# Kernel optimization log

Hardware: AMD Instinct MI355X
Metric: run time of the kernel (lower is better)

The kernel has to match this reference:

```python
import jax, jax.numpy as jnp
import numpy as np
import math

N = 50000      # nodes (single node type 'mapping_var')
D = 128        # in_feats
R = 3          # relations
E = 800000     # edges per relation
OUT = 64
ALPHA = 0.5
BETA1 = math.log(2.0)    # log(lambda/layer + 1), layer=1, lambda=1
BETA2 = math.log(1.5)    # layer=2
SLOPE = 0.01             # leaky_relu default negative slope


def setup_inputs() -> dict:
    key = jax.random.key(0)
    ks = jax.random.split(key, 8)
    x = jax.random.normal(ks[0], (N, D), dtype=jnp.float32)
    src = jax.random.randint(ks[1], (R, E), 0, N, dtype=jnp.int32)
    dst = jax.random.randint(ks[2], (R, E), 0, N, dtype=jnp.int32)
    W1 = jax.random.normal(ks[3], (R, D, D), dtype=jnp.float32) * 0.05
    b1 = jnp.zeros((R, D), dtype=jnp.float32)
    W2 = jax.random.normal(ks[4], (R, D, D), dtype=jnp.float32) * 0.05
    b2 = jnp.zeros((R, D), dtype=jnp.float32)
    Wlin = jax.random.normal(ks[5], (D, OUT), dtype=jnp.float32) * 0.05
    blin = jnp.zeros((OUT,), dtype=jnp.float32)
    return {"x": x, "src": src, "dst": dst, "W1": W1, "b1": b1,
            "W2": W2, "b2": b2, "Wlin": Wlin, "blin": blin}


def _gcn2_rel(h, feat0, src, dst, W, b, beta, act):
    """One GCN2Conv on one relation. h,feat0: [N,D]; src,dst: [E]."""
    ones = jnp.ones(src.shape, h.dtype)
    deg_out = jnp.maximum(jax.ops.segment_sum(ones, src, num_segments=N), 1.0)
    deg_in = jnp.maximum(jax.ops.segment_sum(ones, dst, num_segments=N), 1.0)
    hs = h * (deg_out ** -0.5)[:, None]              # src-side normalize
    agg = jax.ops.segment_sum(hs[src], dst, num_segments=N)  # SpMM via gather+scatter
    feat = agg * (deg_in ** -0.5)[:, None]           # dst-side normalize
    rst = feat * (1.0 - ALPHA) + ALPHA * feat0       # initial-residual blend
    rst = (1.0 - beta) * rst + beta * (rst @ W) + b  # identity mapping (project_initial_features)
    if act:
        rst = jnp.where(rst >= 0, rst, SLOPE * rst)  # leaky_relu
    return rst


def reference(x, src, dst, W1, b1, W2, b2, Wlin, blin):
    # conv1: per-relation GCN2Conv(layer=1, leaky_relu), mean-aggregate over relations
    h1 = jax.vmap(lambda s, d, w, bb: _gcn2_rel(x, x, s, d, w, bb, BETA1, True))(
        src, dst, W1, b1).mean(axis=0)
    # dropout: eval-mode identity
    # conv2: per-relation GCN2Conv(layer=2, no activation), feat_0 = original inputs
    h2 = jax.vmap(lambda s, d, w, bb: _gcn2_rel(h1, x, s, d, w, bb, BETA2, False))(
        src, dst, W2, b2).mean(axis=0)
    return h2 @ Wlin + blin
```

## Files before the change

### kernel.cpp

```cpp
#include <hip/hip_runtime.h>

#define NN    50000
#define DD    128
#define RR    3
#define EE    800000
#define OUTD  64
#define BKT   128
#define NBK   391
#define CAP   2560
#define CAPB  2560
#define CHUNK 2048
#define NCH   391
#define NPB   3125
#define SETUPB 6250
#define ALPHA_ 0.5f
#define SLOPE_ 0.01f
#define BETA1_ 0.6931471805599453f
#define BETA2_ 0.4054651081081644f

typedef __attribute__((ext_vector_type(8))) short short8;
typedef __attribute__((ext_vector_type(4))) float f32x4;

__device__ __forceinline__ unsigned short f2b(float f) {
    unsigned int u = __builtin_bit_cast(unsigned int, f);
    u += 0x7FFFu + ((u >> 16) & 1u);
    return (unsigned short)(u >> 16);
}
__device__ __forceinline__ unsigned int pack2(float lo, float hi) {
    return (unsigned int)f2b(lo) | ((unsigned int)f2b(hi) << 16);
}
__device__ __forceinline__ float blo(unsigned int w) { return __builtin_bit_cast(float, w << 16); }
__device__ __forceinline__ float bhi(unsigned int w) { return __builtin_bit_cast(float, w & 0xFFFF0000u); }

__global__ __launch_bounds__(256) void bin_kernel(
    const int* __restrict__ src, const int* __restrict__ dst,
    int* __restrict__ bcnt_d, int* __restrict__ bcnt_s,
    int* __restrict__ pairs_d, unsigned short* __restrict__ pairs_s)
{
    __shared__ int hist[NBK];
    __shared__ int lbase[NBK];
    __shared__ int gdelta[NBK];
    __shared__ int lcur[NBK];
    __shared__ unsigned int staging[CHUNK];
    unsigned short* staging16 = (unsigned short*)staging;
    const int tid = threadIdx.x;
    const int blk = blockIdx.x;
    const int phase = (blk >= RR * NCH);
    const int rb = phase ? blk - RR * NCH : blk;
    const int r = rb / NCH;
    const int chunk = rb % NCH;
    const int e0 = chunk * CHUNK;
    const int n = min(CHUNK, EE - e0);
    const int* sp = src + (size_t)r * EE + e0;
    const int* dp = dst + (size_t)r * EE + e0;
    const int* kp = phase ? sp : dp;

    for (int i = tid; i < NBK; i += 256) hist[i] = 0;
    __syncthreads();
    for (int i = tid; i < n; i += 256)
        atomicAdd(&hist[kp[i] >> 7], 1);
    __syncthreads();
    if (tid < 64) {
        int carry = 0;
        for (int c0 = 0; c0 < NBK; c0 += 64) {
            const int idx = c0 + tid;
            const int v = (idx < NBK) ? hist[idx] : 0;
            int incl = v;
            #pragma unroll
            for (int d = 1; d < 64; d <<= 1) {
                const int t = __shfl_up(incl, d, 64);
                if (tid >= d) incl += t;
            }
            if (idx < NBK) lbase[idx] = carry + incl - v;
            carry += __shfl(incl, 63, 64);
        }
    }
    __syncthreads();
    if (!phase) {
        for (int b = tid; b < NBK; b += 256) {
            lcur[b] = lbase[b];
            const int h = hist[b];
            if (h > 0) {
                const int gstart = (r * NBK + b) * CAP + atomicAdd(&bcnt_d[r * NBK + b], h);
                gdelta[b] = gstart - lbase[b];
            }
        }
        __syncthreads();
        for (int i = tid; i < n; i += 256) {
            const int d = dp[i];
            const int b = d >> 7;
            const int pos = atomicAdd(&lcur[b], 1);
            staging[pos] = (unsigned int)sp[i] | ((unsigned int)(d & 127) << 16)
                         | ((unsigned int)b << 23);
        }
        __syncthreads();
        for (int j = tid; j < n; j += 256) {
            const unsigned int v = staging[j];
            const int b = v >> 23;
            const int gi = gdelta[b] + j;
            const int lo = gi - (r * NBK + b) * CAP;
            if (lo < CAP) pairs_d[gi] = (int)(v & 0x7FFFFF);
        }
    } else {
        for (int b = tid; b < NBK; b += 256) {
            lcur[b] = lbase[b];
            const int h = hist[b];
            if (h > 0) {
                const int gstart = (r * NBK + b) * CAPB + atomicAdd(&bcnt_s[r * NBK + b], h);
                gdelta[b] = gstart - lbase[b];
            }
        }
        __syncthreads();
        for (int i = tid; i < n; i += 256) {
            const int s = sp[i];
            const int b = s >> 7;
            const int pos = atomicAdd(&lcur[b], 1);
            staging16[pos] = (unsigned short)((b << 7) | (s & 127));
        }
        __syncthreads();
        for (int j = tid; j < n; j += 256) {
            const unsigned short v = staging16[j];
            const int b = v >> 7;
            const int gi = gdelta[b] + j;
            const int lo = gi - (r * NBK + b) * CAPB;
            if (lo < CAPB) pairs_s[gi] = v;
        }
    }
}

__global__ __launch_bounds__(256) void dego_setup_kernel(
    const unsigned short* __restrict__ pairs_s, const int* __restrict__ bcnt_s,
    float* __restrict__ dego_r,
    const float* __restrict__ x, unsigned short* __restrict__ xb,
    const float* __restrict__ W1, const float* __restrict__ W2,
    const float* __restrict__ Wlin, unsigned short* __restrict__ Wt1,
    unsigned short* __restrict__ Wt2, unsigned short* __restrict__ WlT)
{
    __shared__ int scnt[BKT];
    const int tid = threadIdx.x;
    const int blk = blockIdx.x;
    if (blk < RR * NBK) {
        const int n2 = min(bcnt_s[blk], CAPB);
        const unsigned short* ps = pairs_s + (size_t)blk * CAPB;
        if (tid < BKT) scnt[tid] = 0;
        __syncthreads();
        for (int i = tid; i < n2; i += 256)
            atomicAdd(&scnt[ps[i] & 127], 1);
        __syncthreads();
        if (tid < BKT) {
            const int r = blk / NBK;
            const int g = (blk % NBK) * BKT + tid;
            if (g < NN)
                dego_r[r * NN + g] = rsqrtf((float)max(scnt[tid], 1));
        }
    } else {
        const int i = (blk - RR * NBK) * 256 + tid;
        {
            const float4 v = ((const float4*)x)[i];
            ushort4 o;
            o.x = f2b(v.x); o.y = f2b(v.y); o.z = f2b(v.z); o.w = f2b(v.w);
            ((ushort4*)xb)[i] = o;
        }
        if (i < RR * DD * DD) {
            const int r = i >> 14, rem = i & 16383, nn = rem >> 7, k = rem & 127;
            const float diag = (k == nn) ? 1.0f : 0.0f;
            const float w1 = W1[r * DD * DD + k * DD + nn];
            Wt1[i] = f2b(BETA1_ * w1 + diag * (1.0f - BETA1_));
            const float w2 = W2[r * DD * DD + k * DD + nn];
            Wt2[i] = f2b((BETA2_ * w2 + diag * (1.0f - BETA2_)) * (1.0f / 3.0f));
        } else if (i < RR * DD * DD + OUTD * DD) {
            const int j = i - RR * DD * DD;
            const int nn = j >> 7, k = j & 127;
            WlT[j] = f2b(Wlin[k * OUTD + nn]);
        }
    }
}

__global__ __launch_bounds__(256) void sort_kernel(
    int* __restrict__ pairs_d, const int* __restrict__ bcnt_d,
    const float* __restrict__ dego_r,
    int* __restrict__ off_g, int* __restrict__ cnt_g, float* __restrict__ degi_r)
{
    __shared__ int stage[CAP];
    __shared__ int cnt[BKT];
    __shared__ int base[BKT];
    __shared__ int pos[BKT];
    const int tid = threadIdx.x;
    const int bid = blockIdx.x;
    const int rr = bid / NBK;
    const int n = min(bcnt_d[bid], CAP);
    int* pp = pairs_d + (size_t)bid * CAP;
    const float* dego = dego_r + (size_t)rr * NN;
    if (tid < BKT) cnt[tid] = 0;
    __syncthreads();
    for (int i = tid; i < n; i += 256) {
        const int p = pp[i];
        stage[i] = p;
        atomicAdd(&cnt[p >> 16], 1);
    }
    __syncthreads();
    if (tid < 64) {
        int carry = 0;
        for (int c0 = 0; c0 < BKT; c0 += 64) {
            const int v = cnt[c0 + tid];
            int incl = v;
            #pragma unroll
            for (int d = 1; d < 64; d <<= 1) {
                const int t = __shfl_up(incl, d, 64);
                if (tid >= d) incl += t;
            }
            base[c0 + tid] = carry + incl - v;
            carry += __shfl(incl, 63, 64);
        }
    }
    __syncthreads();
    if (tid < BKT) {
        pos[tid] = base[tid];
        const int g = (bid % NBK) * BKT + tid;
        if (g < NN) {
            off_g[rr * NN + g] = bid * CAP + base[tid];
            cnt_g[rr * NN + g] = cnt[tid];
            degi_r[rr * NN + g] = rsqrtf((float)max(cnt[tid], 1));
        }
    }
    __syncthreads();
    for (int i = tid; i < n; i += 256) {
        const int p = stage[i];
        const int q = atomicAdd(&pos[p >> 16], 1);
        const int s = p & 0xFFFF;
        pp[q] = s | ((int)f2b(dego[s]) << 16);
    }
}

__global__ __launch_bounds__(256) void pull_all_kernel(
    const unsigned short* __restrict__ hb,
    const unsigned short* __restrict__ xb,
    const int* __restrict__ csrw, const int* __restrict__ off_g,
    const int* __restrict__ cnt_g, const float* __restrict__ degi_r,
    unsigned short* __restrict__ aggb)
{
    const int blk = blockIdx.x;
    const int r = blk / NPB;
    const int node = (blk % NPB) * 16 + (threadIdx.x >> 4);
    const int lane = threadIdx.x & 15;
    const int gi = r * NN + node;
    const int j0 = off_g[gi];
    const int j1 = j0 + cnt_g[gi];
    const uint4* hb4 = (const uint4*)hb;
    float a0 = 0.f, a1 = 0.f, a2 = 0.f, a3 = 0.f, a4 = 0.f, a5 = 0.f, a6 = 0.f, a7 = 0.f;
    int j = j0;
    for (; j + 4 <= j1; j += 4) {
        const unsigned int p0 = csrw[j],     p1 = csrw[j + 1];
        const unsigned int p2 = csrw[j + 2], p3 = csrw[j + 3];
        const float n0 = bhi(p0), n1 = bhi(p1), n2 = bhi(p2), n3 = bhi(p3);
        const uint4 q0 = hb4[(size_t)(p0 & 0xFFFF) * 16 + lane];
        const uint4 q1 = hb4[(size_t)(p1 & 0xFFFF) * 16 + lane];
        const uint4 q2 = hb4[(size_t)(p2 & 0xFFFF) * 16 + lane];
        const uint4 q3 = hb4[(size_t)(p3 & 0xFFFF) * 16 + lane];
        a0 += blo(q0.x) * n0 + blo(q1.x) * n1 + blo(q2.x) * n2 + blo(q3.x) * n3;
        a1 += bhi(q0.x) * n0 + bhi(q1.x) * n1 + bhi(q2.x) * n2 + bhi(q3.x) * n3;
        a2 += blo(q0.y) * n0 + blo(q1.y) * n1 + blo(q2.y) * n2 + blo(q3.y) * n3;
        a3 += bhi(q0.y) * n0 + bhi(q1.y) * n1 + bhi(q2.y) * n2 + bhi(q3.y) * n3;
        a4 += blo(q0.z) * n0 + blo(q1.z) * n1 + blo(q2.z) * n2 + blo(q3.z) * n3;
        a5 += bhi(q0.z) * n0 + bhi(q1.z) * n1 + bhi(q2.z) * n2 + bhi(q3.z) * n3;
        a6 += blo(q0.w) * n0 + blo(q1.w) * n1 + blo(q2.w) * n2 + blo(q3.w) * n3;
        a7 += bhi(q0.w) * n0 + bhi(q1.w) * n1 + bhi(q2.w) * n2 + bhi(q3.w) * n3;
    }
    for (; j < j1; ++j) {
        const unsigned int p0 = csrw[j];
        const float n0 = bhi(p0);
        const uint4 q0 = hb4[(size_t)(p0 & 0xFFFF) * 16 + lane];
        a0 += blo(q0.x) * n0; a1 += bhi(q0.x) * n0;
        a2 += blo(q0.y) * n0; a3 += bhi(q0.y) * n0;
        a4 += blo(q0.z) * n0; a5 += bhi(q0.z) * n0;
        a6 += blo(q0.w) * n0; a7 += bhi(q0.w) * n0;
    }
    const float nd = degi_r[gi] * (1.0f - ALPHA_);
    const uint4 xq = ((const uint4*)xb)[(size_t)node * 16 + lane];
    uint4 o;
    o.x = pack2(a0 * nd + ALPHA_ * blo(xq.x), a1 * nd + ALPHA_ * bhi(xq.x));
    o.y = pack2(a2 * nd + ALPHA_ * blo(xq.y), a3 * nd + ALPHA_ * bhi(xq.y));
    o.z = pack2(a4 * nd + ALPHA_ * blo(xq.z), a5 * nd + ALPHA_ * bhi(xq.z));
    o.w = pack2(a6 * nd + ALPHA_ * blo(xq.w), a7 * nd + ALPHA_ * bhi(xq.w));
    ((uint4*)aggb)[(size_t)gi * 16 + lane] = o;
}

template<int LIN>
__global__ __launch_bounds__(256) void conv_mfma_kernel(
    const unsigned short* __restrict__ aggb,
    const unsigned short* __restrict__ WtG,
    const float* __restrict__ bias,
    const unsigned short* __restrict__ WlT,
    const float* __restrict__ blin,
    unsigned short* __restrict__ houtb,
    float* __restrict__ outf)
{
    __shared__ unsigned short WtL[DD * 136];
    uint4* WtL4 = (uint4*)WtL;
    const int tid  = threadIdx.x;
    const int wave = tid >> 6;
    const int lane = tid & 63;
    const int l15  = lane & 15;
    const int q    = lane >> 4;
    const int blockRow = blockIdx.x * 64;
    const int row0 = blockRow + wave * 16;
    const int arow = min(row0 + l15, NN - 1);

    f32x4 o[8];
    if (LIN) {
        #pragma unroll
        for (int ct = 0; ct < 8; ++ct) {
            const int col = ct * 16 + l15;
            const float bv = (bias[col] + bias[DD + col] + bias[2 * DD + col]) * (1.0f / 3.0f);
            o[ct] = (f32x4){bv, bv, bv, bv};
        }
    } else {
        #pragma unroll
        for (int ct = 0; ct < 8; ++ct) o[ct] = (f32x4){0.f, 0.f, 0.f, 0.f};
    }

    for (int r = 0; r < RR; ++r) {
        __syncthreads();
        const uint4* wg = (const uint4*)(WtG + (size_t)r * DD * DD);
        for (int i = tid; i < DD * 16; i += 256)
            WtL4[(i >> 4) * 17 + (i & 15)] = wg[i];
        __syncthreads();

        short8 a[4];
        const uint4* ap = (const uint4*)aggb + ((size_t)r * NN + arow) * 16 + q;
        #pragma unroll
        for (int ks = 0; ks < 4; ++ks)
            a[ks] = __builtin_bit_cast(short8, ap[ks * 4]);

        #pragma unroll
        for (int ct = 0; ct < 8; ++ct) {
            f32x4 acc;
            if (LIN) {
                acc = o[ct];
            } else {
                const float bv = bias[r * DD + ct * 16 + l15];
                acc = (f32x4){bv, bv, bv, bv};
            }
            const int nrow = ct * 16 + l15;
            #pragma unroll
            for (int ks = 0; ks < 4; ++ks) {
                const short8 b = __builtin_bit_cast(short8, WtL4[nrow * 17 + ks * 4 + q]);
                acc = __builtin_amdgcn_mfma_f32_16x16x32_bf16(a[ks], b, acc, 0, 0, 0);
            }
            if (LIN) {
                o[ct] = acc;
            } else {
                #pragma unroll
                for (int e = 0; e < 4; ++e) {
                    float v = acc[e];
                    v = v >= 0.f ? v : SLOPE_ * v;
                    o[ct][e] += v * (1.0f / 3.0f);
                }
            }
        }
    }

    __syncthreads();
    unsigned short* tile = WtL;
    #pragma unroll
    for (int ct = 0; ct < 8; ++ct) {
        const int col = ct * 16 + l15;
        #pragma unroll
        for (int e = 0; e < 4; ++e) {
            const int lrow = wave * 16 + q * 4 + e;
            tile[lrow * 136 + col] = f2b(o[ct][e]);
        }
    }
    if (LIN) {
        uint4* wl4 = WtL4 + 64 * 17;
        const uint4* wg = (const uint4*)WlT;
        for (int i = tid; i < OUTD * 16; i += 256)
            wl4[(i >> 4) * 17 + (i & 15)] = wg[i];
    }
    __syncthreads();

    if (!LIN) {
        for (int i = tid; i < 64 * 16; i += 256) {
            const int lrow = i >> 4, c = i & 15;
            const int grow = blockRow + lrow;
            if (grow < NN)
                ((uint4*)houtb)[(size_t)grow * 16 + c] = WtL4[lrow * 17 + c];
        }
    } else {
        short8 a2[4];
        const int lrow = wave * 16 + l15;
        #pragma unroll
        for (int ks = 0; ks < 4; ++ks)
            a2[ks] = __builtin_bit_cast(short8, WtL4[lrow * 17 + ks * 4 + q]);
        #pragma unroll
        for (int ct = 0; ct < 4; ++ct) {
            const int col = ct * 16 + l15;
            const float bv = blin[col];
            f32x4 acc = (f32x4){bv, bv, bv, bv};
            #pragma unroll
            for (int ks = 0; ks < 4; ++ks) {
                const short8 b = __builtin_bit_cast(short8, WtL4[(64 + col) * 17 + ks * 4 + q]);
                acc = __builtin_amdgcn_mfma_f32_16x16x32_bf16(a2[ks], b, acc, 0, 0, 0);
            }
            #pragma unroll
            for (int e = 0; e < 4; ++e) {
                const int grow = row0 + q * 4 + e;
                if (grow < NN) outf[(size_t)grow * OUTD + col] = acc[e];
            }
        }
    }
}

extern "C" void kernel_launch(void* const* d_in, const int* in_sizes, int n_in,
                              void* d_out, int out_size, void* d_ws, size_t ws_size,
                              hipStream_t stream)
{
    const float* x    = (const float*)d_in[0];
    const int*   src  = (const int*)  d_in[1];
    const int*   dst  = (const int*)  d_in[2];
    const float* W1   = (const float*)d_in[3];
    const float* b1   = (const float*)d_in[4];
    const float* W2   = (const float*)d_in[5];
    const float* b2   = (const float*)d_in[6];
    const float* Wlin = (const float*)d_in[7];
    const float* blin = (const float*)d_in[8];
    float* out = (float*)d_out;

    int*   bcnt_d  = (int*)d_ws;
    int*   bcnt_s  = bcnt_d + RR * NBK;
    float* dego_r  = (float*)(bcnt_s + RR * NBK);
    float* degi_r  = dego_r + RR * NN;
    int*   off_g   = (int*)(degi_r + RR * NN);
    int*   cnt_g   = off_g + RR * NN;
    int*   pairs_d = cnt_g + RR * NN + 2;
    unsigned short* pairs_s = (unsigned short*)(pairs_d + (size_t)RR * NBK * CAP);
    unsigned short* xb   = pairs_s + (size_t)RR * NBK * CAPB;
    unsigned short* h1b  = xb + (size_t)NN * DD;
    unsigned short* aggb = h1b + (size_t)NN * DD;
    unsigned short* Wt1  = aggb + (size_t)RR * NN * DD;
    unsigned short* Wt2  = Wt1 + RR * DD * DD;
    unsigned short* WlT  = Wt2 + RR * DD * DD;

    hipMemsetAsync(bcnt_d, 0, (size_t)2 * RR * NBK * sizeof(int), stream);

    const int gemm_blocks = (NN + 63) / 64;

    bin_kernel<<<2 * RR * NCH, 256, 0, stream>>>(src, dst, bcnt_d, bcnt_s, pairs_d, pairs_s);
    dego_setup_kernel<<<RR * NBK + SETUPB, 256, 0, stream>>>(
        pairs_s, bcnt_s, dego_r, x, xb, W1, W2, Wlin, Wt1, Wt2, WlT);
    sort_kernel<<<RR * NBK, 256, 0, stream>>>(
        pairs_d, bcnt_d, dego_r, off_g, cnt_g, degi_r);

    pull_all_kernel<<<RR * NPB, 256, 0, stream>>>(
        xb, xb, pairs_d, off_g, cnt_g, degi_r, aggb);
    conv_mfma_kernel<0><<<gemm_blocks, 256, 0, stream>>>(
        aggb, Wt1, b1, nullptr, nullptr, h1b, nullptr);

    pull_all_kernel<<<RR * NPB, 256, 0, stream>>>(
        h1b, xb, pairs_d, off_g, cnt_g, degi_r, aggb);
    conv_mfma_kernel<1><<<gemm_blocks, 256, 0, stream>>>(
        aggb, Wt2, b2, WlT, blin, nullptr, out);
}
```

Measured before the change: 415.5 us.

## Split feature gather into four column passes and prefetch next relation tile in GEMM

The SpMM pull kernel now runs four times per layer, each launch covering a 32-feature slice with 4 threads per node and 64 nodes per block. A smaller per-pass working set of gathered rows should fit better in cache, in exchange for reading the CSR index stream four times and paying extra launch overhead. The conv GEMM kernel also loads the next relation's A fragments before the barrier so that global loads overlap with the current relation's MFMA work, at some register cost.

```diff
diff --git a/kernel.cpp b/kernel.cpp
--- a/kernel.cpp
+++ b/kernel.cpp
@@ -11,7 +11,7 @@
 #define CAPB  2560
 #define CHUNK 2048
 #define NCH   391
-#define NPB   3125
+#define NB64  782
 #define SETUPB 6250
 #define ALPHA_ 0.5f
 #define SLOPE_ 0.01f
@@ -232,31 +232,32 @@
     }
 }
 
-__global__ __launch_bounds__(256) void pull_all_kernel(
+__global__ __launch_bounds__(256) void pull_pass_kernel(
     const unsigned short* __restrict__ hb,
     const unsigned short* __restrict__ xb,
     const int* __restrict__ csrw, const int* __restrict__ off_g,
     const int* __restrict__ cnt_g, const float* __restrict__ degi_r,
-    unsigned short* __restrict__ aggb)
+    unsigned short* __restrict__ aggb, const int pass)
 {
     const int blk = blockIdx.x;
-    const int r = blk / NPB;
-    const int node = (blk % NPB) * 16 + (threadIdx.x >> 4);
-    const int lane = threadIdx.x & 15;
+    const int r = blk / NB64;
+    const int node = (blk % NB64) * 64 + (threadIdx.x >> 2);
+    const int lane4 = threadIdx.x & 3;
+    if (node >= NN) return;
     const int gi = r * NN + node;
     const int j0 = off_g[gi];
     const int j1 = j0 + cnt_g[gi];
-    const uint4* hb4 = (const uint4*)hb;
+    const uint4* hb4 = (const uint4*)hb + pass * 4 + lane4;
     float a0 = 0.f, a1 = 0.f, a2 = 0.f, a3 = 0.f, a4 = 0.f, a5 = 0.f, a6 = 0.f, a7 = 0.f;
     int j = j0;
     for (; j + 4 <= j1; j += 4) {
         const unsigned int p0 = csrw[j],     p1 = csrw[j + 1];
         const unsigned int p2 = csrw[j + 2], p3 = csrw[j + 3];
         const float n0 = bhi(p0), n1 = bhi(p1), n2 = bhi(p2), n3 = bhi(p3);
-        const uint4 q0 = hb4[(size_t)(p0 & 0xFFFF) * 16 + lane];
-        const uint4 q1 = hb4[(size_t)(p1 & 0xFFFF) * 16 + lane];
-        const uint4 q2 = hb4[(size_t)(p2 & 0xFFFF) * 16 + lane];
-        const uint4 q3 = hb4[(size_t)(p3 & 0xFFFF) * 16 + lane];
+        const uint4 q0 = hb4[(size_t)(p0 & 0xFFFF) * 16];
+        const uint4 q1 = hb4[(size_t)(p1 & 0xFFFF) * 16];
+        const uint4 q2 = hb4[(size_t)(p2 & 0xFFFF) * 16];
+        const uint4 q3 = hb4[(size_t)(p3 & 0xFFFF) * 16];
         a0 += blo(q0.x) * n0 + blo(q1.x) * n1 + blo(q2.x) * n2 + blo(q3.x) * n3;
         a1 += bhi(q0.x) * n0 + bhi(q1.x) * n1 + bhi(q2.x) * n2 + bhi(q3.x) * n3;
         a2 += blo(q0.y) * n0 + blo(q1.y) * n1 + blo(q2.y) * n2 + blo(q3.y) * n3;
@@ -269,20 +270,20 @@
     for (; j < j1; ++j) {
         const unsigned int p0 = csrw[j];
         const float n0 = bhi(p0);
-        const uint4 q0 = hb4[(size_t)(p0 & 0xFFFF) * 16 + lane];
+        const uint4 q0 = hb4[(size_t)(p0 & 0xFFFF) * 16];
         a0 += blo(q0.x) * n0; a1 += bhi(q0.x) * n0;
         a2 += blo(q0.y) * n0; a3 += bhi(q0.y) * n0;
         a4 += blo(q0.z) * n0; a5 += bhi(q0.z) * n0;
         a6 += blo(q0.w) * n0; a7 += bhi(q0.w) * n0;
     }
     const float nd = degi_r[gi] * (1.0f - ALPHA_);
-    const uint4 xq = ((const uint4*)xb)[(size_t)node * 16 + lane];
+    const uint4 xq = ((const uint4*)xb)[(size_t)node * 16 + pass * 4 + lane4];
     uint4 o;
     o.x = pack2(a0 * nd + ALPHA_ * blo(xq.x), a1 * nd + ALPHA_ * bhi(xq.x));
     o.y = pack2(a2 * nd + ALPHA_ * blo(xq.y), a3 * nd + ALPHA_ * bhi(xq.y));
     o.z = pack2(a4 * nd + ALPHA_ * blo(xq.z), a5 * nd + ALPHA_ * bhi(xq.z));
     o.w = pack2(a6 * nd + ALPHA_ * blo(xq.w), a7 * nd + ALPHA_ * bhi(xq.w));
-    ((uint4*)aggb)[(size_t)gi * 16 + lane] = o;
+    ((uint4*)aggb)[(size_t)gi * 16 + pass * 4 + lane4] = o;
 }
 
 template<int LIN>
@@ -319,18 +320,26 @@
         for (int ct = 0; ct < 8; ++ct) o[ct] = (f32x4){0.f, 0.f, 0.f, 0.f};
     }
 
+    short8 a_cur[4], a_nxt[4];
+    {
+        const uint4* ap = (const uint4*)aggb + (size_t)arow * 16 + q;
+        #pragma unroll
+        for (int ks = 0; ks < 4; ++ks)
+            a_cur[ks] = __builtin_bit_cast(short8, ap[ks * 4]);
+    }
+
     for (int r = 0; r < RR; ++r) {
         __syncthreads();
         const uint4* wg = (const uint4*)(WtG + (size_t)r * DD * DD);
         for (int i = tid; i < DD * 16; i += 256)
             WtL4[(i >> 4) * 17 + (i & 15)] = wg[i];
-        __syncthreads();
-
-        short8 a[4];
-        const uint4* ap = (const uint4*)aggb + ((size_t)r * NN + arow) * 16 + q;
-        #pragma unroll
-        for (int ks = 0; ks < 4; ++ks)
-            a[ks] = __builtin_bit_cast(short8, ap[ks * 4]);
+        if (r + 1 < RR) {
+            const uint4* ap = (const uint4*)aggb + ((size_t)(r + 1) * NN + arow) * 16 + q;
+            #pragma unroll
+            for (int ks = 0; ks < 4; ++ks)
+                a_nxt[ks] = __builtin_bit_cast(short8, ap[ks * 4]);
+        }
+        __syncthreads();
 
         #pragma unroll
         for (int ct = 0; ct < 8; ++ct) {
@@ -345,7 +354,7 @@
             #pragma unroll
             for (int ks = 0; ks < 4; ++ks) {
                 const short8 b = __builtin_bit_cast(short8, WtL4[nrow * 17 + ks * 4 + q]);
-                acc = __builtin_amdgcn_mfma_f32_16x16x32_bf16(a[ks], b, acc, 0, 0, 0);
+                acc = __builtin_amdgcn_mfma_f32_16x16x32_bf16(a_cur[ks], b, acc, 0, 0, 0);
             }
             if (LIN) {
                 o[ct] = acc;
@@ -358,6 +367,8 @@
                 }
             }
         }
+        #pragma unroll
+        for (int ks = 0; ks < 4; ++ks) a_cur[ks] = a_nxt[ks];
     }
 
     __syncthreads();
@@ -451,13 +462,15 @@
     sort_kernel<<<RR * NBK, 256, 0, stream>>>(
         pairs_d, bcnt_d, dego_r, off_g, cnt_g, degi_r);
 
-    pull_all_kernel<<<RR * NPB, 256, 0, stream>>>(
-        xb, xb, pairs_d, off_g, cnt_g, degi_r, aggb);
+    for (int p = 0; p < 4; ++p)
+        pull_pass_kernel<<<RR * NB64, 256, 0, stream>>>(
+            xb, xb, pairs_d, off_g, cnt_g, degi_r, aggb, p);
     conv_mfma_kernel<0><<<gemm_blocks, 256, 0, stream>>>(
         aggb, Wt1, b1, nullptr, nullptr, h1b, nullptr);
 
-    pull_all_kernel<<<RR * NPB, 256, 0, stream>>>(
-        h1b, xb, pairs_d, off_g, cnt_g, degi_r, aggb);
+    for (int p = 0; p < 4; ++p)
+        pull_pass_kernel<<<RR * NB64, 256, 0, stream>>>(
+            h1b, xb, pairs_d, off_g, cnt_g, degi_r, aggb, p);
     conv_mfma_kernel<1><<<gemm_blocks, 256, 0, stream>>>(
         aggb, Wt2, b2, WlT, blin, nullptr, out);
 }
```

Result: slower. 669.4 us (+61.1%).

## Fuse neighbor aggregation into MFMA conv kernel and enlarge binning chunks

Applied to the files above, without the earlier changes.

Merges the per-relation gather/aggregate kernel with the MFMA projection kernel. Each 1024-thread block gathers its 64 rows into shared memory per relation, then runs the GEMM from LDS. This removes the intermediate aggregated-feature buffer writes and reads and two kernel launches. It also enlarges the edge-binning chunk size, which reduces the bin kernel's block count. The larger blocks and higher LDS use may reduce occupancy and latency hiding in the gather phase.

```diff
diff --git a/kernel.cpp b/kernel.cpp
--- a/kernel.cpp
+++ b/kernel.cpp
@@ -9,9 +9,8 @@
 #define NBK   391
 #define CAP   2560
 #define CAPB  2560
-#define CHUNK 2048
-#define NCH   391
-#define NPB   3125
+#define CHUNK 8192
+#define NCH   98
 #define SETUPB 6250
 #define ALPHA_ 0.5f
 #define SLOPE_ 0.01f
@@ -20,6 +19,7 @@
 
 typedef __attribute__((ext_vector_type(8))) short short8;
 typedef __attribute__((ext_vector_type(4))) float f32x4;
+typedef __attribute__((ext_vector_type(4))) unsigned int u32x4;
 
 __device__ __forceinline__ unsigned short f2b(float f) {
     unsigned int u = __builtin_bit_cast(unsigned int, f);
@@ -232,62 +232,12 @@
     }
 }
 
-__global__ __launch_bounds__(256) void pull_all_kernel(
+template<int LIN>
+__global__ __launch_bounds__(1024, 8) void pullconv_kernel(
     const unsigned short* __restrict__ hb,
     const unsigned short* __restrict__ xb,
     const int* __restrict__ csrw, const int* __restrict__ off_g,
     const int* __restrict__ cnt_g, const float* __restrict__ degi_r,
-    unsigned short* __restrict__ aggb)
-{
-    const int blk = blockIdx.x;
-    const int r = blk / NPB;
-    const int node = (blk % NPB) * 16 + (threadIdx.x >> 4);
-    const int lane = threadIdx.x & 15;
-    const int gi = r * NN + node;
-    const int j0 = off_g[gi];
-    const int j1 = j0 + cnt_g[gi];
-    const uint4* hb4 = (const uint4*)hb;
-    float a0 = 0.f, a1 = 0.f, a2 = 0.f, a3 = 0.f, a4 = 0.f, a5 = 0.f, a6 = 0.f, a7 = 0.f;
-    int j = j0;
-    for (; j + 4 <= j1; j += 4) {
-        const unsigned int p0 = csrw[j],     p1 = csrw[j + 1];
-        const unsigned int p2 = csrw[j + 2], p3 = csrw[j + 3];
-        const float n0 = bhi(p0), n1 = bhi(p1), n2 = bhi(p2), n3 = bhi(p3);
-        const uint4 q0 = hb4[(size_t)(p0 & 0xFFFF) * 16 + lane];
-        const uint4 q1 = hb4[(size_t)(p1 & 0xFFFF) * 16 + lane];
-        const uint4 q2 = hb4[(size_t)(p2 & 0xFFFF) * 16 + lane];
-        const uint4 q3 = hb4[(size_t)(p3 & 0xFFFF) * 16 + lane];
-        a0 += blo(q0.x) * n0 + blo(q1.x) * n1 + blo(q2.x) * n2 + blo(q3.x) * n3;
-        a1 += bhi(q0.x) * n0 + bhi(q1.x) * n1 + bhi(q2.x) * n2 + bhi(q3.x) * n3;
-        a2 += blo(q0.y) * n0 + blo(q1.y) * n1 + blo(q2.y) * n2 + blo(q3.y) * n3;
-        a3 += bhi(q0.y) * n0 + bhi(q1.y) * n1 + bhi(q2.y) * n2 + bhi(q3.y) * n3;
-        a4 += blo(q0.z) * n0 + blo(q1.z) * n1 + blo(q2.z) * n2 + blo(q3.z) * n3;
-        a5 += bhi(q0.z) * n0 + bhi(q1.z) * n1 + bhi(q2.z) * n2 + bhi(q3.z) * n3;
-        a6 += blo(q0.w) * n0 + blo(q1.w) * n1 + blo(q2.w) * n2 + blo(q3.w) * n3;
-        a7 += bhi(q0.w) * n0 + bhi(q1.w) * n1 + bhi(q2.w) * n2 + bhi(q3.w) * n3;
-    }
-    for (; j < j1; ++j) {
-        const unsigned int p0 = csrw[j];
-        const float n0 = bhi(p0);
-        const uint4 q0 = hb4[(size_t)(p0 & 0xFFFF) * 16 + lane];
-        a0 += blo(q0.x) * n0; a1 += bhi(q0.x) * n0;
-        a2 += blo(q0.y) * n0; a3 += bhi(q0.y) * n0;
-        a4 += blo(q0.z) * n0; a5 += bhi(q0.z) * n0;
-        a6 += blo(q0.w) * n0; a7 += bhi(q0.w) * n0;
-    }
-    const float nd = degi_r[gi] * (1.0f - ALPHA_);
-    const uint4 xq = ((const uint4*)xb)[(size_t)node * 16 + lane];
-    uint4 o;
-    o.x = pack2(a0 * nd + ALPHA_ * blo(xq.x), a1 * nd + ALPHA_ * bhi(xq.x));
-    o.y = pack2(a2 * nd + ALPHA_ * blo(xq.y), a3 * nd + ALPHA_ * bhi(xq.y));
-    o.z = pack2(a4 * nd + ALPHA_ * blo(xq.z), a5 * nd + ALPHA_ * bhi(xq.z));
-    o.w = pack2(a6 * nd + ALPHA_ * blo(xq.w), a7 * nd + ALPHA_ * bhi(xq.w));
-    ((uint4*)aggb)[(size_t)gi * 16 + lane] = o;
-}
-
-template<int LIN>
-__global__ __launch_bounds__(256) void conv_mfma_kernel(
-    const unsigned short* __restrict__ aggb,
     const unsigned short* __restrict__ WtG,
     const float* __restrict__ bias,
     const unsigned short* __restrict__ WlT,
@@ -295,48 +245,99 @@
     unsigned short* __restrict__ houtb,
     float* __restrict__ outf)
 {
+    __shared__ unsigned short AtL[64 * 136];
     __shared__ unsigned short WtL[DD * 136];
+    uint4* AtL4 = (uint4*)AtL;
     uint4* WtL4 = (uint4*)WtL;
-    const int tid  = threadIdx.x;
+    const int tid = threadIdx.x;
+    const int blockRow = blockIdx.x * 64;
+    const int gnode = tid >> 4;
+    const int glane = tid & 15;
+    const int gRowC = min(blockRow + gnode, NN - 1);
     const int wave = tid >> 6;
     const int lane = tid & 63;
     const int l15  = lane & 15;
     const int q    = lane >> 4;
-    const int blockRow = blockIdx.x * 64;
-    const int row0 = blockRow + wave * 16;
-    const int arow = min(row0 + l15, NN - 1);
-
-    f32x4 o[8];
+    const int rg   = wave >> 2;
+    const int cp   = wave & 3;
+    const int arowL = rg * 16 + l15;
+
+    f32x4 o[2];
     if (LIN) {
         #pragma unroll
-        for (int ct = 0; ct < 8; ++ct) {
-            const int col = ct * 16 + l15;
+        for (int ct2 = 0; ct2 < 2; ++ct2) {
+            const int col = (cp * 2 + ct2) * 16 + l15;
             const float bv = (bias[col] + bias[DD + col] + bias[2 * DD + col]) * (1.0f / 3.0f);
-            o[ct] = (f32x4){bv, bv, bv, bv};
+            o[ct2] = (f32x4){bv, bv, bv, bv};
         }
     } else {
-        #pragma unroll
-        for (int ct = 0; ct < 8; ++ct) o[ct] = (f32x4){0.f, 0.f, 0.f, 0.f};
-    }
+        o[0] = (f32x4){0.f, 0.f, 0.f, 0.f};
+        o[1] = (f32x4){0.f, 0.f, 0.f, 0.f};
+    }
+
+    const u32x4* hb4 = (const u32x4*)hb;
 
     for (int r = 0; r < RR; ++r) {
         __syncthreads();
-        const uint4* wg = (const uint4*)(WtG + (size_t)r * DD * DD);
-        for (int i = tid; i < DD * 16; i += 256)
-            WtL4[(i >> 4) * 17 + (i & 15)] = wg[i];
+        {
+            const uint4* wg = (const uint4*)(WtG + (size_t)r * DD * DD);
+            #pragma unroll
+            for (int i = tid; i < DD * 16; i += 1024)
+                WtL4[(i >> 4) * 17 + (i & 15)] = wg[i];
+        }
+        const int gi = r * NN + gRowC;
+        const int j0 = off_g[gi];
+        const int j1 = j0 + cnt_g[gi];
+        float a0 = 0.f, a1 = 0.f, a2 = 0.f, a3 = 0.f, a4 = 0.f, a5 = 0.f, a6 = 0.f, a7 = 0.f;
+        int j = j0;
+        for (; j + 4 <= j1; j += 4) {
+            const unsigned int p0 = csrw[j],     p1 = csrw[j + 1];
+            const unsigned int p2 = csrw[j + 2], p3 = csrw[j + 3];
+            const float n0 = bhi(p0), n1 = bhi(p1), n2 = bhi(p2), n3 = bhi(p3);
+            const u32x4 q0 = hb4[(size_t)(p0 & 0xFFFF) * 16 + glane];
+            const u32x4 q1 = hb4[(size_t)(p1 & 0xFFFF) * 16 + glane];
+            const u32x4 q2 = hb4[(size_t)(p2 & 0xFFFF) * 16 + glane];
+            const u32x4 q3 = hb4[(size_t)(p3 & 0xFFFF) * 16 + glane];
+            a0 += blo(q0.x) * n0 + blo(q1.x) * n1 + blo(q2.x) * n2 + blo(q3.x) * n3;
+            a1 += bhi(q0.x) * n0 + bhi(q1.x) * n1 + bhi(q2.x) * n2 + bhi(q3.x) * n3;
+            a2 += blo(q0.y) * n0 + blo(q1.y) * n1 + blo(q2.y) * n2 + blo(q3.y) * n3;
+            a3 += bhi(q0.y) * n0 + bhi(q1.y) * n1 + bhi(q2.y) * n2 + bhi(q3.y) * n3;
+            a4 += blo(q0.z) * n0 + blo(q1.z) * n1 + blo(q2.z) * n2 + blo(q3.z) * n3;
+            a5 += bhi(q0.z) * n0 + bhi(q1.z) * n1 + bhi(q2.z) * n2 + bhi(q3.z) * n3;
+            a6 += blo(q0.w) * n0 + blo(q1.w) * n1 + blo(q2.w) * n2 + blo(q3.w) * n3;
+            a7 += bhi(q0.w) * n0 + bhi(q1.w) * n1 + bhi(q2.w) * n2 + bhi(q3.w) * n3;
+        }
+        for (; j < j1; ++j) {
+            const unsigned int p0 = csrw[j];
+            const float n0 = bhi(p0);
+            const u32x4 q0 = hb4[(size_t)(p0 & 0xFFFF) * 16 + glane];
+            a0 += blo(q0.x) * n0; a1 += bhi(q0.x) * n0;
+            a2 += blo(q0.y) * n0; a3 += bhi(q0.y) * n0;
+            a4 += blo(q0.z) * n0; a5 += bhi(q0.z) * n0;
+            a6 += blo(q0.w) * n0; a7 += bhi(q0.w) * n0;
+        }
+        {
+            const float nd = degi_r[gi] * (1.0f - ALPHA_);
+            const u32x4 xq = ((const u32x4*)xb)[(size_t)gRowC * 16 + glane];
+            uint4 ov;
+            ov.x = pack2(a0 * nd + ALPHA_ * blo(xq.x), a1 * nd + ALPHA_ * bhi(xq.x));
+            ov.y = pack2(a2 * nd + ALPHA_ * blo(xq.y), a3 * nd + ALPHA_ * bhi(xq.y));
+            ov.z = pack2(a4 * nd + ALPHA_ * blo(xq.z), a5 * nd + ALPHA_ * bhi(xq.z));
+            ov.w = pack2(a6 * nd + ALPHA_ * blo(xq.w), a7 * nd + ALPHA_ * bhi(xq.w));
+            AtL4[gnode * 17 + glane] = ov;
+        }
         __syncthreads();
 
         short8 a[4];
-        const uint4* ap = (const uint4*)aggb + ((size_t)r * NN + arow) * 16 + q;
         #pragma unroll
         for (int ks = 0; ks < 4; ++ks)
-            a[ks] = __builtin_bit_cast(short8, ap[ks * 4]);
-
-        #pragma unroll
-        for (int ct = 0; ct < 8; ++ct) {
+            a[ks] = __builtin_bit_cast(short8, AtL4[arowL * 17 + ks * 4 + q]);
+        #pragma unroll
+        for (int ct2 = 0; ct2 < 2; ++ct2) {
+            const int ct = cp * 2 + ct2;
             f32x4 acc;
             if (LIN) {
-                acc = o[ct];
+                acc = o[ct2];
             } else {
                 const float bv = bias[r * DD + ct * 16 + l15];
                 acc = (f32x4){bv, bv, bv, bv};
@@ -348,65 +349,59 @@
                 acc = __builtin_amdgcn_mfma_f32_16x16x32_bf16(a[ks], b, acc, 0, 0, 0);
             }
             if (LIN) {
-                o[ct] = acc;
+                o[ct2] = acc;
             } else {
                 #pragma unroll
                 for (int e = 0; e < 4; ++e) {
                     float v = acc[e];
                     v = v >= 0.f ? v : SLOPE_ * v;
-                    o[ct][e] += v * (1.0f / 3.0f);
+                    o[ct2][e] += v * (1.0f / 3.0f);
                 }
             }
         }
     }
 
     __syncthreads();
-    unsigned short* tile = WtL;
     #pragma unroll
-    for (int ct = 0; ct < 8; ++ct) {
-        const int col = ct * 16 + l15;
+    for (int ct2 = 0; ct2 < 2; ++ct2) {
+        const int col = (cp * 2 + ct2) * 16 + l15;
         #pragma unroll
         for (int e = 0; e < 4; ++e) {
-            const int lrow = wave * 16 + q * 4 + e;
-            tile[lrow * 136 + col] = f2b(o[ct][e]);
+            const int lrow = rg * 16 + q * 4 + e;
+            AtL[lrow * 136 + col] = f2b(o[ct2][e]);
         }
     }
     if (LIN) {
         uint4* wl4 = WtL4 + 64 * 17;
         const uint4* wg = (const uint4*)WlT;
-        for (int i = tid; i < OUTD * 16; i += 256)
+        #pragma unroll
+        for (int i = tid; i < OUTD * 16; i += 1024)
             wl4[(i >> 4) * 17 + (i & 15)] = wg[i];
     }
     __syncthreads();
 
     if (!LIN) {
-        for (int i = tid; i < 64 * 16; i += 256) {
-            const int lrow = i >> 4, c = i & 15;
-            const int grow = blockRow + lrow;
-            if (grow < NN)
-                ((uint4*)houtb)[(size_t)grow * 16 + c] = WtL4[lrow * 17 + c];
-        }
+        const int lrow = tid >> 4, c = tid & 15;
+        const int grow = blockRow + lrow;
+        if (grow < NN)
+            ((uint4*)houtb)[(size_t)grow * 16 + c] = AtL4[lrow * 17 + c];
     } else {
         short8 a2[4];
-        const int lrow = wave * 16 + l15;
         #pragma unroll
         for (int ks = 0; ks < 4; ++ks)
-            a2[ks] = __builtin_bit_cast(short8, WtL4[lrow * 17 + ks * 4 + q]);
-        #pragma unroll
-        for (int ct = 0; ct < 4; ++ct) {
-            const int col = ct * 16 + l15;
-            const float bv = blin[col];
-            f32x4 acc = (f32x4){bv, bv, bv, bv};
-            #pragma unroll
-            for (int ks = 0; ks < 4; ++ks) {
-                const short8 b = __builtin_bit_cast(short8, WtL4[(64 + col) * 17 + ks * 4 + q]);
-                acc = __builtin_amdgcn_mfma_f32_16x16x32_bf16(a2[ks], b, acc, 0, 0, 0);
-            }
-            #pragma unroll
-            for (int e = 0; e < 4; ++e) {
-                const int grow = row0 + q * 4 + e;
-                if (grow < NN) outf[(size_t)grow * OUTD + col] = acc[e];
-            }
+            a2[ks] = __builtin_bit_cast(short8, AtL4[arowL * 17 + ks * 4 + q]);
+        const int col = cp * 16 + l15;
+        const float bv = blin[col];
+        f32x4 acc = (f32x4){bv, bv, bv, bv};
+        #pragma unroll
+        for (int ks = 0; ks < 4; ++ks) {
+            const short8 b = __builtin_bit_cast(short8, WtL4[(64 + col) * 17 + ks * 4 + q]);
+            acc = __builtin_amdgcn_mfma_f32_16x16x32_bf16(a2[ks], b, acc, 0, 0, 0);
+        }
+        #pragma unroll
+        for (int e = 0; e < 4; ++e) {
+            const int grow = blockRow + rg * 16 + q * 4 + e;
+            if (grow < NN) outf[(size_t)grow * OUTD + col] = acc[e];
         }
     }
 }
@@ -451,13 +446,9 @@
     sort_kernel<<<RR * NBK, 256, 0, stream>>>(
         pairs_d, bcnt_d, dego_r, off_g, cnt_g, degi_r);
 
-    pull_all_kernel<<<RR * NPB, 256, 0, stream>>>(
-        xb, xb, pairs_d, off_g, cnt_g, degi_r, aggb);
-    conv_mfma_kernel<0><<<gemm_blocks, 256, 0, stream>>>(
-        aggb, Wt1, b1, nullptr, nullptr, h1b, nullptr);
-
-    pull_all_kernel<<<RR * NPB, 256, 0, stream>>>(
-        h1b, xb, pairs_d, off_g, cnt_g, degi_r, aggb);
-    conv_mfma_kernel<1><<<gemm_blocks, 256, 0, stream>>>(
-        aggb, Wt2, b2, WlT, blin, nullptr, out);
-}
+    pullconv_kernel<0><<<gemm_blocks, 1024, 0, stream>>>(
+        xb, xb, pairs_d, off_g, cnt_g, degi_r, Wt1, b1, nullptr, nullptr, h1b, nullptr);
+
+    pullconv_kernel<1><<<gemm_blocks, 1024, 0, stream>>>(
+        h1b, xb, pairs_d, off_g, cnt_g, degi_r, Wt2, b2, WlT, blin, nullptr, out);
+}
```

Measured after the change: 409.8 us. No clear change (-1.4%).
